# Performance work log

Hardware: AMD Instinct MI355X
Metric: run time of the kernel (lower is better)

## Reference

```python
import jax, jax.numpy as jnp
import numpy as np

N_NODES = 100000
N_EDGES = 400000
N_GRAPHS = 4096
F_IN, HID, HEADS, OUT_DIM = 64, 64, 4, 128
NEG_SLOPE = 0.2


def gat_layer(x, src, dst, W, a_s, a_d, b, concat):
    # x: [N, Fin]; W: [Fin, H*C]; a_s/a_d: [H, C]; src/dst: [Etot] (self loops included)
    N = x.shape[0]
    H, C = a_s.shape
    h = (x @ W).reshape(N, H, C)
    e_src = jnp.einsum('nhc,hc->nh', h, a_s)  # [N, H]
    e_dst = jnp.einsum('nhc,hc->nh', h, a_d)
    e = jax.nn.leaky_relu(e_src[src] + e_dst[dst], NEG_SLOPE)  # [Etot, H]
    # segment softmax over edges grouped by destination node
    m = jax.ops.segment_max(e, dst, num_segments=N)
    m = jnp.where(jnp.isfinite(m), m, 0.0)
    ex = jnp.exp(e - m[dst])
    denom = jax.ops.segment_sum(ex, dst, num_segments=N)
    alpha = ex / jnp.maximum(denom[dst], 1e-16)  # [Etot, H]
    out = jax.ops.segment_sum(alpha[:, :, None] * h[src], dst, num_segments=N)  # [N, H, C]
    out = out.reshape(N, H * C) if concat else out.mean(axis=1)
    return out + b


def setup_inputs() -> dict:
    key = jax.random.key(0)
    ks = jax.random.split(key, 32)
    x = jax.random.normal(ks[0], (N_NODES, F_IN), dtype=jnp.float32)
    edge_index = jax.random.randint(ks[1], (2, N_EDGES), 0, N_NODES, dtype=jnp.int64) if jax.config.jax_enable_x64 else jax.random.randint(ks[1], (2, N_EDGES), 0, N_NODES).astype(jnp.int32)
    batch = jnp.sort(jax.random.randint(ks[2], (N_NODES,), 0, N_GRAPHS)).astype(edge_index.dtype)
    s = 0.1
    d = {
        'x': x, 'edge_index': edge_index, 'batch': batch, 'num_graphs': N_GRAPHS,
        'W0': jax.random.normal(ks[3], (F_IN, HEADS * HID), jnp.float32) * s,
        'as0': jax.random.normal(ks[4], (HEADS, HID), jnp.float32) * s,
        'ad0': jax.random.normal(ks[5], (HEADS, HID), jnp.float32) * s,
        'b0': jnp.zeros((HEADS * HID,), jnp.float32),
        'W1': jax.random.normal(ks[6], (HEADS * HID, HEADS * HID), jnp.float32) * s,
        'as1': jax.random.normal(ks[7], (HEADS, HID), jnp.float32) * s,
        'ad1': jax.random.normal(ks[8], (HEADS, HID), jnp.float32) * s,
        'b1': jnp.zeros((HEADS * HID,), jnp.float32),
        'W2': jax.random.normal(ks[9], (HEADS * HID, HEADS * HID), jnp.float32) * s,
        'as2': jax.random.normal(ks[10], (HEADS, HID), jnp.float32) * s,
        'ad2': jax.random.normal(ks[11], (HEADS, HID), jnp.float32) * s,
        'b2': jnp.zeros((HEADS * HID,), jnp.float32),
        'W3': jax.random.normal(ks[12], (HEADS * HID, OUT_DIM), jnp.float32) * s,
        'as3': jax.random.normal(ks[13], (1, OUT_DIM), jnp.float32) * s,
        'ad3': jax.random.normal(ks[14], (1, OUT_DIM), jnp.float32) * s,
        'b3': jnp.zeros((OUT_DIM,), jnp.float32),
        'mW0': jax.random.normal(ks[15], (OUT_DIM, OUT_DIM // 2), jnp.float32) * s,
        'mb0': jnp.zeros((OUT_DIM // 2,), jnp.float32),
        'mW1': jax.random.normal(ks[16], (OUT_DIM // 2, OUT_DIM // 4), jnp.float32) * s,
        'mb1': jnp.zeros((OUT_DIM // 4,), jnp.float32),
        'mW2': jax.random.normal(ks[17], (OUT_DIM // 4, 4), jnp.float32) * s,
        'mb2': jnp.zeros((4,), jnp.float32),
    }
    return d


def reference(x, edge_index, batch, num_graphs, W0, as0, ad0, b0, W1, as1, ad1, b1,
              W2, as2, ad2, b2, W3, as3, ad3, b3, mW0, mb0, mW1, mb1, mW2, mb2):
    N = x.shape[0]
    # PyG GATConv default add_self_loops=True
    loop = jnp.arange(N, dtype=edge_index.dtype)
    src = jnp.concatenate([edge_index[0], loop])
    dst = jnp.concatenate([edge_index[1], loop])
    # dropout layers are identity in eval mode
    h = gat_layer(x, src, dst, W0, as0, ad0, b0, concat=True)
    h = jax.nn.elu(h)
    h = gat_layer(h, src, dst, W1, as1, ad1, b1, concat=True)
    h = jax.nn.elu(h)
    h = gat_layer(h, src, dst, W2, as2, ad2, b2, concat=True)
    h = jax.nn.elu(h)
    h = gat_layer(h, src, dst, W3, as3, ad3, b3, concat=False)  # [N, OUT_DIM]
    # global mean pool per graph
    sums = jax.ops.segment_sum(h, batch, num_segments=num_graphs)
    cnt = jax.ops.segment_sum(jnp.ones((N,), h.dtype), batch, num_segments=num_graphs)
    pooled = sums / jnp.maximum(cnt, 1.0)[:, None]  # [G, OUT_DIM]
    # MLPReadout(out_dim, 4, L=2): 128 -> 64 -> 32 -> 4 with ReLU between
    y = jax.nn.relu(pooled @ mW0 + mb0)
    y = jax.nn.relu(y @ mW1 + mb1)
    y = y @ mW2 + mb2
    return y
```

## Files before the change

### kernel.cpp

```cpp
#include <hip/hip_runtime.h>
#include <math.h>

#define N_NODES 100000
#define N_EDGES 400000
#define N_GRAPHS_C 4096
#define E_TOT (N_EDGES + N_NODES)

static inline int ceil_div(int a, int b) { return (a + b - 1) / b; }

typedef __attribute__((ext_vector_type(8))) short short8v;
typedef __attribute__((ext_vector_type(4))) float float4v;

__device__ __forceinline__ float b2f(unsigned short u) {
  union { unsigned int i; float f; } v;
  v.i = ((unsigned int)u) << 16;
  return v.f;
}
__device__ __forceinline__ unsigned short f2b(float f) {
  union { float f; unsigned int i; } v;
  v.f = f;
  unsigned int x = v.i;
  unsigned int r = x + 0x7fffu + ((x >> 16) & 1u);
  return (unsigned short)(r >> 16);
}


__global__ __launch_bounds__(256) void k_cvt_x(const float* __restrict__ in, unsigned short* __restrict__ out,
                                               int n4) {
  int i = blockIdx.x * 256 + threadIdx.x;
  if (i >= n4) return;
  float4 v = *(const float4*)(in + (size_t)i * 4);
  ushort4 o;
  o.x = f2b(v.x); o.y = f2b(v.y); o.z = f2b(v.z); o.w = f2b(v.w);
  *(ushort4*)(out + (size_t)i * 4) = o;
}

__device__ __forceinline__ void cvt_one(const float* __restrict__ W, unsigned short* __restrict__ Wt,
                                        int K, int Ncol, int idx) {
  int n = idx / K, k = idx % K;
  Wt[(size_t)n * K + k] = f2b(W[(size_t)k * Ncol + n]);
}

__global__ __launch_bounds__(256) void k_cvt_w_all(const float* __restrict__ W0, unsigned short* __restrict__ wt0,
                                                   const float* __restrict__ W1, unsigned short* __restrict__ wt1,
                                                   const float* __restrict__ W2, unsigned short* __restrict__ wt2,
                                                   const float* __restrict__ W3, unsigned short* __restrict__ wt3) {
  int i = blockIdx.x * 256 + threadIdx.x;
  const int s0 = 64 * 256, s1 = s0 + 256 * 256, s2 = s1 + 256 * 256, s3 = s2 + 256 * 128;
  if (i < s0) cvt_one(W0, wt0, 64, 256, i);
  else if (i < s1) cvt_one(W1, wt1, 256, 256, i - s0);
  else if (i < s2) cvt_one(W2, wt2, 256, 256, i - s1);
  else if (i < s3) cvt_one(W3, wt3, 256, 128, i - s2);
}


__global__ __launch_bounds__(256) void k_count_deg_g(const int* __restrict__ ei, int* __restrict__ deg,
                                                     const int* __restrict__ batch, int* __restrict__ gcnt) {
  int i = blockIdx.x * 256 + threadIdx.x;
  if (i < N_EDGES) atomicAdd(&deg[ei[N_EDGES + i]], 1);
  if (i < N_NODES) atomicAdd(&gcnt[batch[i]], 1);
}

__global__ __launch_bounds__(256) void k_scan(int* __restrict__ deg, int* __restrict__ offs,
                                              int* __restrict__ cursor, int* __restrict__ counter) {
  __shared__ int sm[256];
  __shared__ int sbase;
  int tid = threadIdx.x;
  int n = blockIdx.x * 256 + tid;
  int d = (n < N_NODES) ? (deg[n] + 1) : 0;
  sm[tid] = d;
  __syncthreads();
  for (int off = 1; off < 256; off <<= 1) {
    int v = (tid >= off) ? sm[tid - off] : 0;
    __syncthreads();
    sm[tid] += v;
    __syncthreads();
  }
  if (tid == 255) sbase = atomicAdd(counter, sm[255]);
  __syncthreads();
  int excl = sm[tid] - d;
  if (n < N_NODES) {
    int o = sbase + excl;
    offs[n] = o;
    cursor[n] = o;
    deg[n] = d;
  }
}

__global__ __launch_bounds__(256) void k_scatter(const int* __restrict__ ei, int* __restrict__ cursor,
                                                 int* __restrict__ csr) {
  int i = blockIdx.x * 256 + threadIdx.x;
  if (i < N_EDGES) {
    int d = ei[N_EDGES + i];
    int pos = atomicAdd(&cursor[d], 1);
    csr[pos] = ei[i];
  } else if (i < E_TOT) {
    int n = i - N_EDGES;
    int pos = atomicAdd(&cursor[n], 1);
    csr[pos] = n;
  }
}

__global__ __launch_bounds__(256) void k_gscan(const int* __restrict__ gcnt, int* __restrict__ gptr) {
  __shared__ int sm[256];
  __shared__ int srun;
  int tid = threadIdx.x;
  if (tid == 0) srun = 0;
  __syncthreads();
  for (int c = 0; c < N_GRAPHS_C / 256; c++) {
    int idx = c * 256 + tid;
    int v = gcnt[idx];
    sm[tid] = v;
    __syncthreads();
    for (int off = 1; off < 256; off <<= 1) {
      int t = (tid >= off) ? sm[tid - off] : 0;
      __syncthreads();
      sm[tid] += t;
      __syncthreads();
    }
    gptr[idx] = srun + sm[tid] - v;
    __syncthreads();
    if (tid == 0) srun += sm[255];
    __syncthreads();
  }
}


#define LDA 40

template <int ATT>
__global__ __launch_bounds__(256) void k_gemm_bf16(const unsigned short* __restrict__ A,
                                                   const unsigned short* __restrict__ Wt,
                                                   unsigned short* __restrict__ out, int M, int K, int Ncol,
                                                   const float* __restrict__ a_s, const float* __restrict__ a_d,
                                                   float* __restrict__ es, float* __restrict__ ed) {
  __shared__ unsigned short As[128 * LDA];
  __shared__ unsigned short Bs[128 * LDA];
  int tid = threadIdx.x;
  int wave = tid >> 6, lane = tid & 63;
  int quad = lane >> 4, l16 = lane & 15;
  int wrow = (wave & 1) * 64, wcol = (wave >> 1) * 64;
  int row0 = blockIdx.x * 128, col0 = blockIdx.y * 128;

  float4v acc[4][4];
#pragma unroll
  for (int i = 0; i < 4; i++)
#pragma unroll
    for (int j = 0; j < 4; j++) acc[i][j] = (float4v)(0.f);

  int r0 = tid >> 2, c0 = (tid & 3) * 8;
  int r1 = (tid + 256) >> 2, c1 = c0;

  for (int k0 = 0; k0 < K; k0 += 32) {
    uint4 a0 = make_uint4(0, 0, 0, 0), a1 = make_uint4(0, 0, 0, 0);
    if (row0 + r0 < M) a0 = *(const uint4*)(A + (size_t)(row0 + r0) * K + k0 + c0);
    if (row0 + r1 < M) a1 = *(const uint4*)(A + (size_t)(row0 + r1) * K + k0 + c1);
    uint4 b0 = *(const uint4*)(Wt + (size_t)(col0 + r0) * K + k0 + c0);
    uint4 b1 = *(const uint4*)(Wt + (size_t)(col0 + r1) * K + k0 + c1);
    __syncthreads();
    *(uint4*)(&As[r0 * LDA + c0]) = a0;
    *(uint4*)(&As[r1 * LDA + c1]) = a1;
    *(uint4*)(&Bs[r0 * LDA + c0]) = b0;
    *(uint4*)(&Bs[r1 * LDA + c1]) = b1;
    __syncthreads();

    short8v af[4], bf[4];
#pragma unroll
    for (int i = 0; i < 4; i++)
      af[i] = *(const short8v*)(&As[(wrow + i * 16 + l16) * LDA + quad * 8]);
#pragma unroll
    for (int j = 0; j < 4; j++)
      bf[j] = *(const short8v*)(&Bs[(wcol + j * 16 + l16) * LDA + quad * 8]);
#pragma unroll
    for (int i = 0; i < 4; i++)
#pragma unroll
      for (int j = 0; j < 4; j++)
        acc[i][j] = __builtin_amdgcn_mfma_f32_16x16x32_bf16(af[i], bf[j], acc[i][j], 0, 0, 0);
  }

#pragma unroll
  for (int i = 0; i < 4; i++) {
#pragma unroll
    for (int r = 0; r < 4; r++) {
      int m = row0 + wrow + i * 16 + quad * 4 + r;
      if (m < M) {
#pragma unroll
        for (int j = 0; j < 4; j++) {
          int col = col0 + wcol + j * 16 + l16;
          out[(size_t)m * Ncol + col] = f2b(acc[i][j][r]);
        }
      }
    }
  }

  if (ATT == 1) {
    int h = (col0 + wcol) >> 6;
    float as_r[4], ad_r[4];
#pragma unroll
    for (int j = 0; j < 4; j++) {
      as_r[j] = a_s[h * 64 + j * 16 + l16];
      ad_r[j] = a_d[h * 64 + j * 16 + l16];
    }
#pragma unroll
    for (int i = 0; i < 4; i++) {
#pragma unroll
      for (int r = 0; r < 4; r++) {
        float pes = acc[i][0][r] * as_r[0] + acc[i][1][r] * as_r[1] + acc[i][2][r] * as_r[2] + acc[i][3][r] * as_r[3];
        float ped = acc[i][0][r] * ad_r[0] + acc[i][1][r] * ad_r[1] + acc[i][2][r] * ad_r[2] + acc[i][3][r] * ad_r[3];
#pragma unroll
        for (int mk = 1; mk < 16; mk <<= 1) {
          pes += __shfl_xor(pes, mk, 64);
          ped += __shfl_xor(ped, mk, 64);
        }
        if (l16 == 0) {
          int m = row0 + wrow + i * 16 + quad * 4 + r;
          if (m < M) {
            es[m * 4 + h] = pes;
            ed[m * 4 + h] = ped;
          }
        }
      }
    }
  }

  if (ATT == 2) {
    __shared__ float ps[128][2], pd[128][2];
    float as_r[4], ad_r[4];
#pragma unroll
    for (int j = 0; j < 4; j++) {
      as_r[j] = a_s[wcol + j * 16 + l16];
      ad_r[j] = a_d[wcol + j * 16 + l16];
    }
#pragma unroll
    for (int i = 0; i < 4; i++) {
#pragma unroll
      for (int r = 0; r < 4; r++) {
        float pes = acc[i][0][r] * as_r[0] + acc[i][1][r] * as_r[1] + acc[i][2][r] * as_r[2] + acc[i][3][r] * as_r[3];
        float ped = acc[i][0][r] * ad_r[0] + acc[i][1][r] * ad_r[1] + acc[i][2][r] * ad_r[2] + acc[i][3][r] * ad_r[3];
#pragma unroll
        for (int mk = 1; mk < 16; mk <<= 1) {
          pes += __shfl_xor(pes, mk, 64);
          ped += __shfl_xor(ped, mk, 64);
        }
        if (l16 == 0) {
          int lr = wrow + i * 16 + quad * 4 + r;
          ps[lr][wcol >> 6] = pes;
          pd[lr][wcol >> 6] = ped;
        }
      }
    }
    __syncthreads();
    if (tid < 128) {
      int m = row0 + tid;
      if (m < M) {
        es[m] = ps[tid][0] + ps[tid][1];
        ed[m] = pd[tid][0] + pd[tid][1];
      }
    }
  }
}


template <int H>
__global__ __launch_bounds__(256) void k_logits_stats(const float* __restrict__ es, const float* __restrict__ ed,
                                                      const int* __restrict__ csr, const int* __restrict__ offs,
                                                      const int* __restrict__ deg, float* __restrict__ ew) {
  int idx = blockIdx.x * 256 + threadIdx.x;
  if (idx >= N_NODES * H) return;
  int n = (H == 1) ? idx : (idx >> 2);
  int h = (H == 1) ? 0 : (idx & 3);
  int start = offs[n];
  int c = deg[n];
  const int* csrp = csr + start;
  float* p = ew + (size_t)start * H + h;
  float edn = ed[n * H + h];

  float m = -1e30f;
  for (int i = 0; i < c; i++) {
    int s = csrp[i];
    float e = es[s * H + h] + edn;
    e = e > 0.f ? e : 0.2f * e;
    p[(size_t)i * H] = e;
    m = fmaxf(m, e);
  }
  float sum = 0.f;
  for (int i = 0; i < c; i++) sum += __expf(p[(size_t)i * H] - m);
  float inv = 1.0f / fmaxf(sum, 1e-16f);
  for (int i = 0; i < c; i++) p[(size_t)i * H] = __expf(p[(size_t)i * H] - m) * inv;
}


__device__ __forceinline__ void acc4(float* acc, float w, uint2 u) {
  acc[0] += w * b2f((unsigned short)(u.x & 0xffff));
  acc[1] += w * b2f((unsigned short)(u.x >> 16));
  acc[2] += w * b2f((unsigned short)(u.y & 0xffff));
  acc[3] += w * b2f((unsigned short)(u.y >> 16));
}
__device__ __forceinline__ void acc2(float* acc, float w, unsigned int u) {
  acc[0] += w * b2f((unsigned short)(u & 0xffff));
  acc[1] += w * b2f((unsigned short)(u >> 16));
}

template <int H, int C>
__global__ __launch_bounds__(256) void k_aggregate(const unsigned short* __restrict__ hbuf,
                                                   const float* __restrict__ ew,
                                                   const int* __restrict__ offs, const int* __restrict__ deg,
                                                   const int* __restrict__ csr, const float* __restrict__ bias,
                                                   unsigned short* __restrict__ out, int applyElu) {
  constexpr int F = H * C;
  constexpr int VPL = F / 64;
  int wave = threadIdx.x >> 6;
  int lane = threadIdx.x & 63;
  int n = blockIdx.x * 4 + wave;
  if (n >= N_NODES) return;
  int head = (H == 1) ? 0 : (lane >> 4);
  int start = offs[n];
  int cnt = deg[n];
  const float* ewp = ew + (size_t)start * H + head;
  const int* csrp = csr + start;

  float acc[VPL];
#pragma unroll
  for (int j = 0; j < VPL; j++) acc[j] = 0.f;

  int i = 0;
  for (; i + 4 <= cnt; i += 4) {
    int s0 = csrp[i], s1 = csrp[i + 1], s2 = csrp[i + 2], s3 = csrp[i + 3];
    float w0 = ewp[(size_t)(i + 0) * H];
    float w1 = ewp[(size_t)(i + 1) * H];
    float w2 = ewp[(size_t)(i + 2) * H];
    float w3 = ewp[(size_t)(i + 3) * H];
    if (VPL == 4) {
      uint2 u0 = *(const uint2*)(hbuf + (size_t)s0 * F + lane * 4);
      uint2 u1 = *(const uint2*)(hbuf + (size_t)s1 * F + lane * 4);
      uint2 u2 = *(const uint2*)(hbuf + (size_t)s2 * F + lane * 4);
      uint2 u3 = *(const uint2*)(hbuf + (size_t)s3 * F + lane * 4);
      acc4(acc, w0, u0); acc4(acc, w1, u1); acc4(acc, w2, u2); acc4(acc, w3, u3);
    } else {
      unsigned int u0 = *(const unsigned int*)(hbuf + (size_t)s0 * F + lane * 2);
      unsigned int u1 = *(const unsigned int*)(hbuf + (size_t)s1 * F + lane * 2);
      unsigned int u2 = *(const unsigned int*)(hbuf + (size_t)s2 * F + lane * 2);
      unsigned int u3 = *(const unsigned int*)(hbuf + (size_t)s3 * F + lane * 2);
      acc2(acc, w0, u0); acc2(acc, w1, u1); acc2(acc, w2, u2); acc2(acc, w3, u3);
    }
  }
  for (; i < cnt; i++) {
    int s = csrp[i];
    float w = ewp[(size_t)i * H];
    if (VPL == 4) {
      uint2 u = *(const uint2*)(hbuf + (size_t)s * F + lane * 4);
      acc4(acc, w, u);
    } else {
      unsigned int u = *(const unsigned int*)(hbuf + (size_t)s * F + lane * 2);
      acc2(acc, w, u);
    }
  }

  unsigned short ob[VPL];
#pragma unroll
  for (int j = 0; j < VPL; j++) {
    float v = acc[j] + bias[lane * VPL + j];
    if (applyElu) v = v > 0.f ? v : expm1f(v);
    ob[j] = f2b(v);
  }
  if (VPL == 4) {
    ushort4 o = make_ushort4(ob[0], ob[1], ob[2], ob[3]);
    *(ushort4*)(out + (size_t)n * F + lane * 4) = o;
  } else {
    ushort2 o = make_ushort2(ob[0], ob[1]);
    *(ushort2*)(out + (size_t)n * F + lane * 2) = o;
  }
}


__global__ __launch_bounds__(128) void k_pool_readout(const unsigned short* __restrict__ feat,
                                                      const int* __restrict__ gptr, const int* __restrict__ gcnt,
                                                      const float* __restrict__ mW0, const float* __restrict__ mb0,
                                                      const float* __restrict__ mW1, const float* __restrict__ mb1,
                                                      const float* __restrict__ mW2, const float* __restrict__ mb2,
                                                      float* __restrict__ out) {
  __shared__ float p[128];
  __shared__ float y1[64];
  __shared__ float y2[32];
  int g = blockIdx.x;
  int t = threadIdx.x;
  int start = gptr[g];
  int c = gcnt[g];
  float a = 0.f;
  for (int i = 0; i < c; i++) a += b2f(feat[(size_t)(start + i) * 128 + t]);
  p[t] = a / fmaxf((float)c, 1.0f);
  __syncthreads();
  if (t < 64) {
    float v = mb0[t];
#pragma unroll 4
    for (int k = 0; k < 128; k++) v += p[k] * mW0[k * 64 + t];
    y1[t] = v > 0.f ? v : 0.f;
  }
  __syncthreads();
  if (t < 32) {
    float v = mb1[t];
#pragma unroll 4
    for (int k = 0; k < 64; k++) v += y1[k] * mW1[k * 32 + t];
    y2[t] = v > 0.f ? v : 0.f;
  }
  __syncthreads();
  if (t < 4) {
    float v = mb2[t];
#pragma unroll 4
    for (int k = 0; k < 32; k++) v += y2[k] * mW2[k * 4 + t];
    out[(size_t)g * 4 + t] = v;
  }
}


extern "C" void kernel_launch(void* const* d_in, const int* in_sizes, int n_in,
                              void* d_out, int out_size, void* d_ws, size_t ws_size,
                              hipStream_t stream) {
  const float* x = (const float*)d_in[0];
  const int* ei = (const int*)d_in[1];
  const int* batch = (const int*)d_in[2];
  const float* W0 = (const float*)d_in[4];
  const float* as0 = (const float*)d_in[5];
  const float* ad0 = (const float*)d_in[6];
  const float* b0 = (const float*)d_in[7];
  const float* W1 = (const float*)d_in[8];
  const float* as1 = (const float*)d_in[9];
  const float* ad1 = (const float*)d_in[10];
  const float* b1 = (const float*)d_in[11];
  const float* W2 = (const float*)d_in[12];
  const float* as2 = (const float*)d_in[13];
  const float* ad2 = (const float*)d_in[14];
  const float* b2 = (const float*)d_in[15];
  const float* W3 = (const float*)d_in[16];
  const float* as3 = (const float*)d_in[17];
  const float* ad3 = (const float*)d_in[18];
  const float* b3 = (const float*)d_in[19];
  const float* mW0 = (const float*)d_in[20];
  const float* mb0 = (const float*)d_in[21];
  const float* mW1 = (const float*)d_in[22];
  const float* mb1 = (const float*)d_in[23];
  const float* mW2 = (const float*)d_in[24];
  const float* mb2 = (const float*)d_in[25];
  float* out = (float*)d_out;

  char* ws = (char*)d_ws;
  size_t cur = 0;
  auto alloc = [&](size_t bytes) -> char* {
    char* p = ws + cur;
    cur += (bytes + 255) & ~(size_t)255;
    return p;
  };
  unsigned short* featA = (unsigned short*)alloc((size_t)N_NODES * 256 * 2);
  unsigned short* hB = (unsigned short*)alloc((size_t)N_NODES * 256 * 2);
  unsigned short* xb = (unsigned short*)alloc((size_t)N_NODES * 64 * 2);
  unsigned short* wt0 = (unsigned short*)alloc((size_t)256 * 64 * 2);
  unsigned short* wt1 = (unsigned short*)alloc((size_t)256 * 256 * 2);
  unsigned short* wt2 = (unsigned short*)alloc((size_t)256 * 256 * 2);
  unsigned short* wt3 = (unsigned short*)alloc((size_t)128 * 256 * 2);
  float* es = (float*)alloc((size_t)N_NODES * 4 * sizeof(float));
  float* ed = (float*)alloc((size_t)N_NODES * 4 * sizeof(float));
  float* ew = (float*)alloc((size_t)E_TOT * 4 * sizeof(float));
  int* deg = (int*)alloc((size_t)N_NODES * sizeof(int));
  int* counter = (int*)alloc(256);
  int* gcnt = (int*)alloc((size_t)N_GRAPHS_C * sizeof(int));
  size_t zeroBytes = (char*)(gcnt + N_GRAPHS_C) - (char*)deg;
  int* offs = (int*)alloc((size_t)N_NODES * sizeof(int));
  int* cursor = (int*)alloc((size_t)N_NODES * sizeof(int));
  int* csr = (int*)alloc((size_t)E_TOT * sizeof(int));
  int* gptr = (int*)alloc((size_t)N_GRAPHS_C * sizeof(int));
  (void)ws_size; (void)in_sizes; (void)n_in; (void)out_size;

  k_cvt_x<<<ceil_div(N_NODES * 64 / 4, 256), 256, 0, stream>>>(x, xb, N_NODES * 64 / 4);
  k_cvt_w_all<<<ceil_div(64 * 256 + 2 * 256 * 256 + 256 * 128, 256), 256, 0, stream>>>(W0, wt0, W1, wt1, W2, wt2, W3, wt3);

  hipMemsetAsync(deg, 0, zeroBytes, stream);
  k_count_deg_g<<<ceil_div(N_EDGES, 256), 256, 0, stream>>>(ei, deg, batch, gcnt);
  k_scan<<<ceil_div(N_NODES, 256), 256, 0, stream>>>(deg, offs, cursor, counter);
  k_scatter<<<ceil_div(E_TOT, 256), 256, 0, stream>>>(ei, cursor, csr);
  k_gscan<<<1, 256, 0, stream>>>(gcnt, gptr);

  int gm = ceil_div(N_NODES, 128);
  dim3 g256(gm, 2), g128(gm, 1);
  int aggBlocks = ceil_div(N_NODES, 4);
  int lsBlocks4 = ceil_div(N_NODES * 4, 256);
  int lsBlocks1 = ceil_div(N_NODES, 256);

  k_gemm_bf16<1><<<g256, 256, 0, stream>>>(xb, wt0, hB, N_NODES, 64, 256, as0, ad0, es, ed);
  k_logits_stats<4><<<lsBlocks4, 256, 0, stream>>>(es, ed, csr, offs, deg, ew);
  k_aggregate<4, 64><<<aggBlocks, 256, 0, stream>>>(hB, ew, offs, deg, csr, b0, featA, 1);

  k_gemm_bf16<1><<<g256, 256, 0, stream>>>(featA, wt1, hB, N_NODES, 256, 256, as1, ad1, es, ed);
  k_logits_stats<4><<<lsBlocks4, 256, 0, stream>>>(es, ed, csr, offs, deg, ew);
  k_aggregate<4, 64><<<aggBlocks, 256, 0, stream>>>(hB, ew, offs, deg, csr, b1, featA, 1);

  k_gemm_bf16<1><<<g256, 256, 0, stream>>>(featA, wt2, hB, N_NODES, 256, 256, as2, ad2, es, ed);
  k_logits_stats<4><<<lsBlocks4, 256, 0, stream>>>(es, ed, csr, offs, deg, ew);
  k_aggregate<4, 64><<<aggBlocks, 256, 0, stream>>>(hB, ew, offs, deg, csr, b2, featA, 1);

  k_gemm_bf16<2><<<g128, 256, 0, stream>>>(featA, wt3, hB, N_NODES, 256, 128, as3, ad3, es, ed);
  k_logits_stats<1><<<lsBlocks1, 256, 0, stream>>>(es, ed, csr, offs, deg, ew);
  k_aggregate<1, 128><<<aggBlocks, 256, 0, stream>>>(hB, ew, offs, deg, csr, b3, featA, 0);

  k_pool_readout<<<N_GRAPHS_C, 128, 0, stream>>>(featA, gptr, gcnt, mW0, mb0, mW1, mb1, mW2, mb2, out);
}
```

Baseline: 656.3 us.

## Fold attention vectors into GEMM weights as extra columns; cache exp in softmax

Precomputes W·a_s and W·a_d as extra bf16 weight rows, so the attention logits come out of additional MFMA tiles inside the GEMM. This replaces the shuffle-reduction epilogue and, for the last layer, its shared-memory combine. The softmax stats kernel now stores exp values instead of recomputing them, and pool readout sums with two waves and packed bf16 loads. The trade-off is that logits are now computed from bf16-rounded folded weights, which may shift precision slightly, and one wave per extra block does additional MFMA work.

```diff
diff --git a/kernel.cpp b/kernel.cpp
--- a/kernel.cpp
+++ b/kernel.cpp
@@ -51,6 +51,30 @@
   else if (i < s1) cvt_one(W1, wt1, 256, 256, i - s0);
   else if (i < s2) cvt_one(W2, wt2, 256, 256, i - s1);
   else if (i < s3) cvt_one(W3, wt3, 256, 128, i - s2);
+}
+
+__device__ __forceinline__ void wa_one(const float* __restrict__ W, const float* __restrict__ a_s,
+                                       const float* __restrict__ a_d, unsigned short* __restrict__ wt,
+                                       int K, int Ncol, int H, int C, int idx) {
+  int k = idx % K;
+  int j = idx / K;
+  const float* a = (j < H) ? a_s : a_d;
+  int h = (j < H) ? j : j - H;
+  float s = 0.f;
+  for (int c = 0; c < C; c++) s += W[(size_t)k * Ncol + h * C + c] * a[h * C + c];
+  wt[(size_t)(Ncol + j) * K + k] = f2b(s);
+}
+
+__global__ __launch_bounds__(256) void k_cvt_wa(const float* __restrict__ W0, const float* __restrict__ as0, const float* __restrict__ ad0, unsigned short* __restrict__ wt0,
+                                                const float* __restrict__ W1, const float* __restrict__ as1, const float* __restrict__ ad1, unsigned short* __restrict__ wt1,
+                                                const float* __restrict__ W2, const float* __restrict__ as2, const float* __restrict__ ad2, unsigned short* __restrict__ wt2,
+                                                const float* __restrict__ W3, const float* __restrict__ as3, const float* __restrict__ ad3, unsigned short* __restrict__ wt3) {
+  int i = blockIdx.x * 256 + threadIdx.x;
+  const int s0 = 64 * 8, s1 = s0 + 256 * 8, s2 = s1 + 256 * 8, s3 = s2 + 256 * 2;
+  if (i < s0) wa_one(W0, as0, ad0, wt0, 64, 256, 4, 64, i);
+  else if (i < s1) wa_one(W1, as1, ad1, wt1, 256, 256, 4, 64, i - s0);
+  else if (i < s2) wa_one(W2, as2, ad2, wt2, 256, 256, 4, 64, i - s1);
+  else if (i < s3) wa_one(W3, as3, ad3, wt3, 256, 128, 1, 128, i - s2);
 }
 
 
@@ -132,21 +156,27 @@
 __global__ __launch_bounds__(256) void k_gemm_bf16(const unsigned short* __restrict__ A,
                                                    const unsigned short* __restrict__ Wt,
                                                    unsigned short* __restrict__ out, int M, int K, int Ncol,
-                                                   const float* __restrict__ a_s, const float* __restrict__ a_d,
                                                    float* __restrict__ es, float* __restrict__ ed) {
   __shared__ unsigned short As[128 * LDA];
-  __shared__ unsigned short Bs[128 * LDA];
+  __shared__ unsigned short Bs[144 * LDA];
   int tid = threadIdx.x;
   int wave = tid >> 6, lane = tid & 63;
   int quad = lane >> 4, l16 = lane & 15;
   int wrow = (wave & 1) * 64, wcol = (wave >> 1) * 64;
   int row0 = blockIdx.x * 128, col0 = blockIdx.y * 128;
 
+  constexpr int EX = (ATT == 1) ? 8 : ((ATT == 2) ? 2 : 0);
+  bool blockExtra = (ATT == 1) ? (blockIdx.y == 1) : (ATT == 2);
+  bool waveExtra = blockExtra && (wcol == 0);
+
   float4v acc[4][4];
 #pragma unroll
   for (int i = 0; i < 4; i++)
 #pragma unroll
     for (int j = 0; j < 4; j++) acc[i][j] = (float4v)(0.f);
+  float4v acc_e[4];
+#pragma unroll
+  for (int i = 0; i < 4; i++) acc_e[i] = (float4v)(0.f);
 
   int r0 = tid >> 2, c0 = (tid & 3) * 8;
   int r1 = (tid + 256) >> 2, c1 = c0;
@@ -157,11 +187,16 @@
     if (row0 + r1 < M) a1 = *(const uint4*)(A + (size_t)(row0 + r1) * K + k0 + c1);
     uint4 b0 = *(const uint4*)(Wt + (size_t)(col0 + r0) * K + k0 + c0);
     uint4 b1 = *(const uint4*)(Wt + (size_t)(col0 + r1) * K + k0 + c1);
+    uint4 bx = make_uint4(0, 0, 0, 0);
+    if (EX && blockExtra && tid < EX * 4)
+      bx = *(const uint4*)(Wt + (size_t)(Ncol + (tid >> 2)) * K + k0 + c0);
     __syncthreads();
     *(uint4*)(&As[r0 * LDA + c0]) = a0;
     *(uint4*)(&As[r1 * LDA + c1]) = a1;
     *(uint4*)(&Bs[r0 * LDA + c0]) = b0;
     *(uint4*)(&Bs[r1 * LDA + c1]) = b1;
+    if (EX && blockExtra && tid < EX * 4)
+      *(uint4*)(&Bs[(128 + (tid >> 2)) * LDA + c0]) = bx;
     __syncthreads();
 
     short8v af[4], bf[4];
@@ -176,6 +211,12 @@
 #pragma unroll
       for (int j = 0; j < 4; j++)
         acc[i][j] = __builtin_amdgcn_mfma_f32_16x16x32_bf16(af[i], bf[j], acc[i][j], 0, 0, 0);
+    if (EX && waveExtra) {
+      short8v bfe = *(const short8v*)(&Bs[(128 + l16) * LDA + quad * 8]);
+#pragma unroll
+      for (int i = 0; i < 4; i++)
+        acc_e[i] = __builtin_amdgcn_mfma_f32_16x16x32_bf16(af[i], bfe, acc_e[i], 0, 0, 0);
+    }
   }
 
 #pragma unroll
@@ -193,68 +234,16 @@
     }
   }
 
-  if (ATT == 1) {
-    int h = (col0 + wcol) >> 6;
-    float as_r[4], ad_r[4];
-#pragma unroll
-    for (int j = 0; j < 4; j++) {
-      as_r[j] = a_s[h * 64 + j * 16 + l16];
-      ad_r[j] = a_d[h * 64 + j * 16 + l16];
-    }
+  if (EX && waveExtra && l16 < EX) {
+    constexpr int H = (ATT == 1) ? 4 : 1;
+    float* dst = (l16 < H) ? es : ed;
+    int h = (l16 < H) ? l16 : l16 - H;
 #pragma unroll
     for (int i = 0; i < 4; i++) {
 #pragma unroll
       for (int r = 0; r < 4; r++) {
-        float pes = acc[i][0][r] * as_r[0] + acc[i][1][r] * as_r[1] + acc[i][2][r] * as_r[2] + acc[i][3][r] * as_r[3];
-        float ped = acc[i][0][r] * ad_r[0] + acc[i][1][r] * ad_r[1] + acc[i][2][r] * ad_r[2] + acc[i][3][r] * ad_r[3];
-#pragma unroll
-        for (int mk = 1; mk < 16; mk <<= 1) {
-          pes += __shfl_xor(pes, mk, 64);
-          ped += __shfl_xor(ped, mk, 64);
-        }
-        if (l16 == 0) {
-          int m = row0 + wrow + i * 16 + quad * 4 + r;
-          if (m < M) {
-            es[m * 4 + h] = pes;
-            ed[m * 4 + h] = ped;
-          }
-        }
-      }
-    }
-  }
-
-  if (ATT == 2) {
-    __shared__ float ps[128][2], pd[128][2];
-    float as_r[4], ad_r[4];
-#pragma unroll
-    for (int j = 0; j < 4; j++) {
-      as_r[j] = a_s[wcol + j * 16 + l16];
-      ad_r[j] = a_d[wcol + j * 16 + l16];
-    }
-#pragma unroll
-    for (int i = 0; i < 4; i++) {
-#pragma unroll
-      for (int r = 0; r < 4; r++) {
-        float pes = acc[i][0][r] * as_r[0] + acc[i][1][r] * as_r[1] + acc[i][2][r] * as_r[2] + acc[i][3][r] * as_r[3];
-        float ped = acc[i][0][r] * ad_r[0] + acc[i][1][r] * ad_r[1] + acc[i][2][r] * ad_r[2] + acc[i][3][r] * ad_r[3];
-#pragma unroll
-        for (int mk = 1; mk < 16; mk <<= 1) {
-          pes += __shfl_xor(pes, mk, 64);
-          ped += __shfl_xor(ped, mk, 64);
-        }
-        if (l16 == 0) {
-          int lr = wrow + i * 16 + quad * 4 + r;
-          ps[lr][wcol >> 6] = pes;
-          pd[lr][wcol >> 6] = ped;
-        }
-      }
-    }
-    __syncthreads();
-    if (tid < 128) {
-      int m = row0 + tid;
-      if (m < M) {
-        es[m] = ps[tid][0] + ps[tid][1];
-        ed[m] = pd[tid][0] + pd[tid][1];
+        int m = row0 + wrow + i * 16 + quad * 4 + r;
+        if (m < M) dst[m * H + h] = acc_e[i][r];
       }
     }
   }
@@ -284,9 +273,13 @@
     m = fmaxf(m, e);
   }
   float sum = 0.f;
-  for (int i = 0; i < c; i++) sum += __expf(p[(size_t)i * H] - m);
+  for (int i = 0; i < c; i++) {
+    float ex = __expf(p[(size_t)i * H] - m);
+    p[(size_t)i * H] = ex;
+    sum += ex;
+  }
   float inv = 1.0f / fmaxf(sum, 1e-16f);
-  for (int i = 0; i < c; i++) p[(size_t)i * H] = __expf(p[(size_t)i * H] - m) * inv;
+  for (int i = 0; i < c; i++) p[(size_t)i * H] *= inv;
 }
 
 
@@ -379,16 +372,26 @@
                                                       const float* __restrict__ mW1, const float* __restrict__ mb1,
                                                       const float* __restrict__ mW2, const float* __restrict__ mb2,
                                                       float* __restrict__ out) {
+  __shared__ float part[2][128];
   __shared__ float p[128];
   __shared__ float y1[64];
   __shared__ float y2[32];
   int g = blockIdx.x;
   int t = threadIdx.x;
+  int w = t >> 6, lane = t & 63;
   int start = gptr[g];
   int c = gcnt[g];
-  float a = 0.f;
-  for (int i = 0; i < c; i++) a += b2f(feat[(size_t)(start + i) * 128 + t]);
-  p[t] = a / fmaxf((float)c, 1.0f);
+  float a0 = 0.f, a1 = 0.f;
+  for (int i = w; i < c; i += 2) {
+    unsigned int u = *(const unsigned int*)(feat + (size_t)(start + i) * 128 + lane * 2);
+    a0 += b2f((unsigned short)(u & 0xffff));
+    a1 += b2f((unsigned short)(u >> 16));
+  }
+  part[w][lane * 2 + 0] = a0;
+  part[w][lane * 2 + 1] = a1;
+  __syncthreads();
+  float invc = 1.0f / fmaxf((float)c, 1.0f);
+  p[t] = (part[0][t] + part[1][t]) * invc;
   __syncthreads();
   if (t < 64) {
     float v = mb0[t];
@@ -453,10 +456,10 @@
   unsigned short* featA = (unsigned short*)alloc((size_t)N_NODES * 256 * 2);
   unsigned short* hB = (unsigned short*)alloc((size_t)N_NODES * 256 * 2);
   unsigned short* xb = (unsigned short*)alloc((size_t)N_NODES * 64 * 2);
-  unsigned short* wt0 = (unsigned short*)alloc((size_t)256 * 64 * 2);
-  unsigned short* wt1 = (unsigned short*)alloc((size_t)256 * 256 * 2);
-  unsigned short* wt2 = (unsigned short*)alloc((size_t)256 * 256 * 2);
-  unsigned short* wt3 = (unsigned short*)alloc((size_t)128 * 256 * 2);
+  unsigned short* wt0 = (unsigned short*)alloc((size_t)264 * 64 * 2);
+  unsigned short* wt1 = (unsigned short*)alloc((size_t)264 * 256 * 2);
+  unsigned short* wt2 = (unsigned short*)alloc((size_t)264 * 256 * 2);
+  unsigned short* wt3 = (unsigned short*)alloc((size_t)130 * 256 * 2);
   float* es = (float*)alloc((size_t)N_NODES * 4 * sizeof(float));
   float* ed = (float*)alloc((size_t)N_NODES * 4 * sizeof(float));
   float* ew = (float*)alloc((size_t)E_TOT * 4 * sizeof(float));
@@ -472,6 +475,8 @@
 
   k_cvt_x<<<ceil_div(N_NODES * 64 / 4, 256), 256, 0, stream>>>(x, xb, N_NODES * 64 / 4);
   k_cvt_w_all<<<ceil_div(64 * 256 + 2 * 256 * 256 + 256 * 128, 256), 256, 0, stream>>>(W0, wt0, W1, wt1, W2, wt2, W3, wt3);
+  k_cvt_wa<<<ceil_div(64 * 8 + 2 * 256 * 8 + 256 * 2, 256), 256, 0, stream>>>(
+      W0, as0, ad0, wt0, W1, as1, ad1, wt1, W2, as2, ad2, wt2, W3, as3, ad3, wt3);
 
   hipMemsetAsync(deg, 0, zeroBytes, stream);
   k_count_deg_g<<<ceil_div(N_EDGES, 256), 256, 0, stream>>>(ei, deg, batch, gcnt);
@@ -485,19 +490,19 @@
   int lsBlocks4 = ceil_div(N_NODES * 4, 256);
   int lsBlocks1 = ceil_div(N_NODES, 256);
 
-  k_gemm_bf16<1><<<g256, 256, 0, stream>>>(xb, wt0, hB, N_NODES, 64, 256, as0, ad0, es, ed);
+  k_gemm_bf16<1><<<g256, 256, 0, stream>>>(xb, wt0, hB, N_NODES, 64, 256, es, ed);
   k_logits_stats<4><<<lsBlocks4, 256, 0, stream>>>(es, ed, csr, offs, deg, ew);
   k_aggregate<4, 64><<<aggBlocks, 256, 0, stream>>>(hB, ew, offs, deg, csr, b0, featA, 1);
 
-  k_gemm_bf16<1><<<g256, 256, 0, stream>>>(featA, wt1, hB, N_NODES, 256, 256, as1, ad1, es, ed);
+  k_gemm_bf16<1><<<g256, 256, 0, stream>>>(featA, wt1, hB, N_NODES, 256, 256, es, ed);
   k_logits_stats<4><<<lsBlocks4, 256, 0, stream>>>(es, ed, csr, offs, deg, ew);
   k_aggregate<4, 64><<<aggBlocks, 256, 0, stream>>>(hB, ew, offs, deg, csr, b1, featA, 1);
 
-  k_gemm_bf16<1><<<g256, 256, 0, stream>>>(featA, wt2, hB, N_NODES, 256, 256, as2, ad2, es, ed);
+  k_gemm_bf16<1><<<g256, 256, 0, stream>>>(featA, wt2, hB, N_NODES, 256, 256, es, ed);
   k_logits_stats<4><<<lsBlocks4, 256, 0, stream>>>(es, ed, csr, offs, deg, ew);
   k_aggregate<4, 64><<<aggBlocks, 256, 0, stream>>>(hB, ew, offs, deg, csr, b2, featA, 1);
 
-  k_gemm_bf16<2><<<g128, 256, 0, stream>>>(featA, wt3, hB, N_NODES, 256, 128, as3, ad3, es, ed);
+  k_gemm_bf16<2><<<g128, 256, 0, stream>>>(featA, wt3, hB, N_NODES, 256, 128, es, ed);
   k_logits_stats<1><<<lsBlocks1, 256, 0, stream>>>(es, ed, csr, offs, deg, ew);
   k_aggregate<1, 128><<<aggBlocks, 256, 0, stream>>>(hB, ew, offs, deg, csr, b3, featA, 0);
 
```

Measured after the change: 629.5 us. 4.1% less time.
